# Kernel tuning notes

Measured on AMD Instinct MI355X. Metric: run time of the kernel, lower is better.

The kernel has to match this reference:

```python
import jax, jax.numpy as jnp
import numpy as np

SIGMA = 1.0
DELTA = 1.0
TOPK = 10
TOPK_HALF = 5  # int(np.around(TOPK / 2))
N, D = 4096, 512
N_IDS = 2048  # N / view


def _l2_normalize(x, eps=1e-12):
    n = jnp.linalg.norm(x, axis=1, keepdims=True)
    return x / jnp.maximum(n, eps)


def _cdist(a, b):
    # Euclidean distance with a sqrt that is safe at 0 (diagonal).
    sq = (jnp.sum(a * a, 1)[:, None] + jnp.sum(b * b, 1)[None, :]
          - 2.0 * (a @ b.T))
    sq = jnp.maximum(sq, 0.0)
    return jnp.where(sq > 0, jnp.sqrt(jnp.where(sq > 0, sq, 1.0)), 0.0)


def setup_inputs() -> dict:
    key = jax.random.key(0)
    k1, k2, k3 = jax.random.split(key, 3)
    s_emb = jax.random.normal(k1, (N, D), dtype=jnp.float32)
    t_emb = jax.random.normal(k2, (N, D), dtype=jnp.float32)
    idx = jax.random.randint(k3, (N,), 0, N_IDS, dtype=jnp.int64)
    return {"s_emb": s_emb, "t_emb": t_emb, "idx": idx}


def reference(s_emb, t_emb, idx):
    n = s_emb.shape[0]
    s = _l2_normalize(s_emb)          # disable_mu=True
    t = _l2_normalize(t_emb)

    S_dist = _cdist(s, s)
    S_dist = S_dist / jnp.mean(S_dist, axis=1, keepdims=True)

    # --- teacher-side neighbor graph (no_grad in original) ---
    T_dist = _cdist(t, t)
    W_P = jnp.exp(-(T_dist ** 2) / SIGMA)                      # [N,N]
    same = idx[:, None] == idx[None, :]
    W_P_copy = jnp.where(same, 1.0, W_P)
    _, topk_index = jax.lax.top_k(W_P_copy, TOPK)              # [N,k]
    topk_half_index = topk_index[:, :TOPK_HALF]                # [N,k/2]

    rows = jnp.arange(n)[:, None]
    W_NN = jnp.zeros((n, n), jnp.float32).at[rows, topk_index].set(1.0)
    V = ((W_NN + W_NN.T) / 2.0 == 1.0).astype(jnp.float32)     # mutual kNN

    # Vectorized form of the per-row nonzero gather-reduce loop:
    # W_C_tilda[i,j] = V[i,j] * (sum_l V[i,l] V[j,l]) / |{l: V[i,l]>0}|
    row_cnt = jnp.sum(V, axis=1)                               # [N]
    VV = jnp.einsum('il,jl->ij', V, V)                         # [N,N]
    W_C_tilda = jnp.where(V > 0, VV / jnp.maximum(row_cnt, 1.0)[:, None], 0.0)

    W_C_hat = jnp.mean(W_C_tilda[topk_half_index], axis=1)     # [N,k/2,N]->[N,N]
    W_C = (W_C_hat + W_C_hat.T) / 2.0
    W = (W_P + W_C) / 2.0

    eye = jnp.eye(n, dtype=jnp.float32)
    pos_weight = W * (1.0 - eye)
    neg_weight = (1.0 - W) * (1.0 - eye)

    pull = jnp.maximum(S_dist, 0.0) ** 2 * pos_weight
    push = jnp.maximum(DELTA - S_dist, 0.0) ** 2 * neg_weight
    loss = (jnp.sum(pull) + jnp.sum(push)) / (n * (n - 1))
    return loss
```

## Files before the change

### kernel.cpp

```cpp
#include <hip/hip_runtime.h>
#include <math.h>

#define N 4096
#define D 512
#define TOPK 10
#define TOPK_HALF 5
#define NT 32
#define TRI_BLOCKS (NT * (NT + 1) / 2)
#define WC_BLOCKS (N * TOPK_HALF / 16)
#define INV_N (1.0f / 4096.0f)
#define TPAD 132

typedef __bf16 bf16;
typedef __bf16 bf16x4 __attribute__((ext_vector_type(4)));
typedef __bf16 bf16x8 __attribute__((ext_vector_type(8)));
typedef float f32x4 __attribute__((ext_vector_type(4)));
typedef _Float16 f16;
typedef _Float16 f16x4 __attribute__((ext_vector_type(4)));
typedef _Float16 f16x8 __attribute__((ext_vector_type(8)));
typedef unsigned short u16;
typedef unsigned short u16x8 __attribute__((ext_vector_type(8)));
typedef unsigned int u32;

__device__ __forceinline__ void gl_lds16(const void* g, void* l) {
  __builtin_amdgcn_global_load_lds(
      (const __attribute__((address_space(1))) void*)g,
      (__attribute__((address_space(3))) void*)l, 16, 0, 0);
}

__device__ __forceinline__ float f16tof(u16 h) {
  return (float)__builtin_bit_cast(_Float16, h);
}

__global__ __launch_bounds__(256) void k_normalize2(const float* __restrict__ xs,
                                                    const float* __restrict__ xt,
                                                    bf16* __restrict__ ys,
                                                    bf16* __restrict__ yt,
                                                    float* __restrict__ rsq_s,
                                                    float* __restrict__ rsq_t,
                                                    float* __restrict__ rowsum) {
  int b = blockIdx.x;
  int tid = threadIdx.x;
  int half = tid >> 7;
  int l = tid & 127;
  int row2 = 2 * b + half;
  int is_t = row2 >> 12;
  int row = row2 & (N - 1);
  const float* x = is_t ? xt : xs;
  bf16* y = is_t ? yt : ys;
  float* rowsq = is_t ? rsq_t : rsq_s;
  const float* xr = x + (size_t)row * D;
  float4 v = *(const float4*)(xr + l * 4);
  float ss = v.x * v.x + v.y * v.y + v.z * v.z + v.w * v.w;
  __shared__ float red[4];
  __shared__ float red2[4];
  for (int off = 32; off > 0; off >>= 1) ss += __shfl_down(ss, off, 64);
  if ((tid & 63) == 0) red[tid >> 6] = ss;
  __syncthreads();
  float tot = red[half * 2] + red[half * 2 + 1];
  float inv = 1.0f / fmaxf(sqrtf(tot), 1e-12f);
  bf16x4 bv;
  bv[0] = (bf16)(v.x * inv); bv[1] = (bf16)(v.y * inv);
  bv[2] = (bf16)(v.z * inv); bv[3] = (bf16)(v.w * inv);
  *(bf16x4*)(y + (size_t)row * D + l * 4) = bv;
  float f0 = (float)bv[0], f1 = (float)bv[1], f2 = (float)bv[2], f3 = (float)bv[3];
  float s2 = f0 * f0 + f1 * f1 + f2 * f2 + f3 * f3;
  for (int off = 32; off > 0; off >>= 1) s2 += __shfl_down(s2, off, 64);
  if ((tid & 63) == 0) red2[tid >> 6] = s2;
  __syncthreads();
  if ((tid & 127) == 0) {
    rowsq[row] = red2[half * 2] + red2[half * 2 + 1];
    if (!is_t) rowsum[row] = 0.f;
  }
}

__global__ __launch_bounds__(256) void k_dgram3(const bf16* __restrict__ S,
                                                const bf16* __restrict__ T,
                                                const float* __restrict__ rsq_s,
                                                const float* __restrict__ rsq_t,
                                                f16* __restrict__ Gsd,
                                                f16* __restrict__ Gwp,
                                                float* __restrict__ rowsum) {
  __shared__ __align__(16) char sm[33792];
  f16* tp = (f16*)sm;

  int z = blockIdx.y;
  const bf16* Y = z ? T : S;
  const float* rsq = z ? rsq_t : rsq_s;
  f16* G = z ? Gwp : Gsd;

  int orig = blockIdx.x;
  int t = (orig & 7) * (TRI_BLOCKS / 8) + (orig >> 3);
  int by = 0;
  while (t >= NT - by) { t -= NT - by; ++by; }
  int bx = by + t;
  bool offdiag = (bx != by);

  int tid = threadIdx.x;
  int lane = tid & 63, w = tid >> 6;
  int wr = w >> 1, wc = w & 1;
  int quad = lane >> 4, c = lane & 15;

  const char* Jbase = (const char*)(Y + (size_t)(bx * 128) * D);
  const char* Ibase = (const char*)(Y + (size_t)(by * 128) * D);

  int goff[4];
  int ldso[4];
#pragma unroll
  for (int i = 0; i < 4; ++i) {
    int s = i * 256 + tid;
    int r = s >> 3;
    int cs = (tid & 7) ^ (r & 7);
    goff[i] = r * (D * 2) + cs * 16;
    ldso[i] = (i * 256 + w * 64) * 16;
  }

  int jrow = wr * 64 + c;
  int irow = wc * 64 + c;
  int x7 = c & 7;
  int csx0 = ((quad) ^ x7) * 16;
  int csx1 = ((4 + quad) ^ x7) * 16;

  f32x4 acc[4][4] = {};
  for (int tt = 0; tt < 8; ++tt) {
    int kb = tt * 128;
#pragma unroll
    for (int i = 0; i < 4; ++i) gl_lds16(Jbase + goff[i] + kb, sm + ldso[i]);
#pragma unroll
    for (int i = 0; i < 4; ++i) gl_lds16(Ibase + goff[i] + kb, sm + 16384 + ldso[i]);
    asm volatile("s_waitcnt vmcnt(0)\n\ts_barrier" ::: "memory");
    {
      const char* Jc = sm;
      const char* Ic = sm + 16384;
#pragma unroll
      for (int m = 0; m < 2; ++m) {
        int csx = m ? csx1 : csx0;
        bf16x8 af[4], bfr[4];
#pragma unroll
        for (int u = 0; u < 4; ++u)
          af[u] = *(const bf16x8*)(Jc + jrow * 128 + u * 2048 + csx);
#pragma unroll
        for (int v = 0; v < 4; ++v)
          bfr[v] = *(const bf16x8*)(Ic + irow * 128 + v * 2048 + csx);
#pragma unroll
        for (int u = 0; u < 4; ++u)
#pragma unroll
          for (int v = 0; v < 4; ++v)
            acc[u][v] = __builtin_amdgcn_mfma_f32_16x16x32_bf16(
                af[u], bfr[v], acc[u][v], 0, 0, 0);
      }
    }
    asm volatile("s_waitcnt lgkmcnt(0)\n\ts_barrier" ::: "memory");
  }

#pragma unroll
  for (int v = 0; v < 4; ++v) {
    int il = wc * 64 + v * 16 + c;
    int ig = by * 128 + il;
    float ri = rsq[ig];
    float rsv = 0.f;
#pragma unroll
    for (int u = 0; u < 4; ++u) {
      int jl0 = wr * 64 + u * 16 + quad * 4;
      int jb0i = bx * 128 + jl0;
      float4 rj = *(const float4*)(rsq + jb0i);
      const float* rjp = (const float*)&rj;
      f32x4 a = acc[u][v];
      f16x4 st;
      if (z == 0) {
#pragma unroll
        for (int reg = 0; reg < 4; ++reg) {
          float sq = fmaxf(ri + rjp[reg] - 2.0f * a[reg], 0.0f);
          float val = __builtin_amdgcn_sqrtf(sq);
          st[reg] = (_Float16)val;
          rsv += val;
        }
      } else {
#pragma unroll
        for (int reg = 0; reg < 4; ++reg) {
          float sq = fmaxf(ri + rjp[reg] - 2.0f * a[reg], 0.0f);
          st[reg] = (_Float16)__expf(-sq);
        }
      }
      *(f16x4*)(G + (size_t)ig * N + jb0i) = st;
      if (offdiag) {
#pragma unroll
        for (int reg = 0; reg < 4; ++reg) tp[(jl0 + reg) * TPAD + il] = st[reg];
      }
    }
    if (z == 0) {
      rsv += __shfl_xor(rsv, 16, 64);
      rsv += __shfl_xor(rsv, 32, 64);
      if (lane < 16) atomicAdd(&rowsum[ig], rsv);
    }
  }

  if (offdiag) {
    __syncthreads();
    int rloc = tid >> 4;
    int cseg = tid & 15;
#pragma unroll
    for (int it = 0; it < 8; ++it) {
      int jl = it * 16 + rloc;
      int jg = bx * 128 + jl;
      f16x8 v8 = *(f16x8*)&tp[jl * TPAD + cseg * 8];
      *(f16x8*)(G + (size_t)jg * N + by * 128 + cseg * 8) = v8;
      if (z == 0) {
        float csum = 0.f;
#pragma unroll
        for (int e = 0; e < 8; ++e) csum += (float)v8[e];
        csum += __shfl_xor(csum, 1, 64);
        csum += __shfl_xor(csum, 2, 64);
        csum += __shfl_xor(csum, 4, 64);
        csum += __shfl_xor(csum, 8, 64);
        if (cseg == 0) atomicAdd(&rowsum[jg], csum);
      }
    }
  }
}

__global__ __launch_bounds__(256) void k_rowpass(const f16* __restrict__ Gs,
                                                 const f16* __restrict__ Gw,
                                                 const int* __restrict__ ids,
                                                 const float* __restrict__ rowsum,
                                                 int* __restrict__ topk,
                                                 double* __restrict__ pd) {
  __shared__ u32 lds[256 * TOPK];
  __shared__ double dred[4];
  int i = blockIdx.x, tid = threadIdx.x;
  int idi = ids[i];
  float invm = 1.0f / (rowsum[i] * INV_N);
  const u16* srow = (const u16*)(Gs + (size_t)i * N);
  const u16* wrow = (const u16*)(Gw + (size_t)i * N);
  u32 key[16];
  float dsum = 0.f;
  int j0 = tid * 16;
#pragma unroll
  for (int h = 0; h < 2; ++h) {
    int jb = j0 + h * 8;
    u16x8 sv = *(const u16x8*)(srow + jb);
    u16x8 wv = *(const u16x8*)(wrow + jb);
    int4 id0 = *(const int4*)(ids + jb);
    int4 id1 = *(const int4*)(ids + jb + 4);
    const int* idp = (const int*)&id0;
    const int* idp1 = (const int*)&id1;
#pragma unroll
    for (int e = 0; e < 8; ++e) {
      int j = jb + e;
      u16 hw = wv[e];
      float wp = f16tof(hw);
      if (j != i) {
        float sdn = f16tof(sv[e]) * invm;
        float r = fmaxf(1.0f - sdn, 0.0f); r *= r;
        dsum += r + 0.5f * wp * (sdn * sdn - r);
      }
      int idj = (e < 4) ? idp[e] : idp1[e - 4];
      u16 hk = (idj == idi) ? (u16)0x3C00 : hw;
      key[h * 8 + e] = ((u32)hk << 16) | (u32)(4095 - j);
    }
  }
#pragma unroll
  for (int kk = 2; kk <= 16; kk <<= 1) {
#pragma unroll
    for (int jj = kk >> 1; jj > 0; jj >>= 1) {
#pragma unroll
      for (int ii = 0; ii < 16; ++ii) {
        int ll = ii ^ jj;
        if (ll > ii) {
          bool desc = ((ii & kk) == 0);
          u32 a = key[ii], b = key[ll];
          bool sw = desc ? (a < b) : (a > b);
          key[ii] = sw ? b : a;
          key[ll] = sw ? a : b;
        }
      }
    }
  }
  double dl = (double)dsum;
  for (int off = 32; off > 0; off >>= 1) dl += __shfl_down(dl, off, 64);
  if ((tid & 63) == 0) dred[tid >> 6] = dl;
#pragma unroll
  for (int o = 0; o < TOPK; ++o) lds[tid * TOPK + o] = key[o];
  __syncthreads();
  for (int off = 128; off >= 1; off >>= 1) {
    if (tid < off) {
      u32 A[TOPK], B[TOPK];
#pragma unroll
      for (int o = 0; o < TOPK; ++o) {
        A[o] = lds[tid * TOPK + o];
        B[o] = lds[(tid + off) * TOPK + o];
      }
      u32 out[TOPK];
#pragma unroll
      for (int o = 0; o < TOPK; ++o) {
        u32 m = A[o] > B[o] ? A[o] : B[o];
#pragma unroll
        for (int p = 0; p < o; ++p) {
          u32 mn = A[p] < B[o - 1 - p] ? A[p] : B[o - 1 - p];
          m = m > mn ? m : mn;
        }
        out[o] = m;
      }
#pragma unroll
      for (int o = 0; o < TOPK; ++o) lds[tid * TOPK + o] = out[o];
    }
    __syncthreads();
  }
  if (tid == 0) {
#pragma unroll
    for (int o = 0; o < TOPK; ++o)
      topk[i * TOPK + o] = 4095 - (int)(lds[o] & 0xFFFu);
    pd[i] = dred[0] + dred[1] + dred[2] + dred[3];
  }
}

__global__ __launch_bounds__(256) void k_buildV(const int* __restrict__ topk,
                                                int* __restrict__ L,
                                                int* __restrict__ cnt) {
  int tid = threadIdx.x;
  int grp = tid >> 4, gl = tid & 15;
  int i = blockIdx.x * 16 + grp;
  bool act = (gl < TOPK);
  int j = act ? topk[i * TOPK + gl] : 0;
  bool mut = false;
  if (act) {
#pragma unroll
    for (int q = 0; q < TOPK; ++q) mut |= (topk[j * TOPK + q] == i);
  }
  unsigned long long m = __ballot(mut);
  int base = tid & 48;
  unsigned gm = (unsigned)((m >> base) & 0xFFFFull);
  int pos = __popc(gm & ((1u << gl) - 1));
  if (mut) L[i * TOPK + pos] = j;
  if (gl == 0) cnt[i] = __popc(gm);
}

__global__ __launch_bounds__(256) void k_wc(const int* __restrict__ topk,
                                            const int* __restrict__ L,
                                            const int* __restrict__ cnt,
                                            const f16* __restrict__ Gsd,
                                            const float* __restrict__ rowsum,
                                            double* __restrict__ pw) {
  __shared__ double red[16];
  int tid = threadIdx.x;
  int grp = tid >> 4;
  int gl = tid & 15;
  int task = blockIdx.x * 16 + grp;
  int i = task / TOPK_HALF, m = task % TOPK_HALF;
  int r = topk[i * TOPK + m];
  int cr = cnt[r];
  float invmi = 1.0f / (rowsum[i] * INV_N);
  int lval = (gl < cr) ? L[r * TOPK + gl] : -1;
  int Lr[TOPK];
#pragma unroll
  for (int a = 0; a < TOPK; ++a) Lr[a] = __shfl(lval, a, 16);
  float contrib = 0.f;
  if (gl < cr) {
    int j = lval;
    if (j != i) {
      int cj = cnt[j];
      float mj = rowsum[j] * INV_N;
      float sr_ = f16tof(((const u16*)Gsd)[(size_t)i * N + j]);
      int lj[TOPK];
#pragma unroll
      for (int b = 0; b < TOPK; ++b) lj[b] = L[j * TOPK + b];
      int vv = 0;
#pragma unroll
      for (int b = 0; b < TOPK; ++b) {
        if (b < cj) {
#pragma unroll
          for (int a = 0; a < TOPK; ++a)
            vv += ((a < cr) && (lj[b] == Lr[a])) ? 1 : 0;
        }
      }
      float denom = (float)(cr > 1 ? cr : 1);
      float wgt = (float)vv / denom;
      float sdij = sr_ * invmi;
      float sdji = sr_ / mj;
      float Rij = fmaxf(1.0f - sdij, 0.0f); Rij *= Rij;
      float Rji = fmaxf(1.0f - sdji, 0.0f); Rji *= Rji;
      float Fij = sdij * sdij - Rij;
      float Fji = sdji * sdji - Rji;
      contrib = wgt * (Fij + Fji);
    }
  }
  double local = (double)contrib;
  local += __shfl_xor(local, 1, 16);
  local += __shfl_xor(local, 2, 16);
  local += __shfl_xor(local, 4, 16);
  local += __shfl_xor(local, 8, 16);
  if (gl == 0) red[grp] = local;
  __syncthreads();
  if (tid == 0) {
    double s = 0.0;
#pragma unroll
    for (int g = 0; g < 16; ++g) s += red[g];
    pw[blockIdx.x] = s * (1.0 / 20.0);
  }
}

__global__ __launch_bounds__(256) void k_final(const double* __restrict__ pd,
                                               const double* __restrict__ pw,
                                               float* __restrict__ out) {
  int tid = threadIdx.x;
  double s = 0.0;
  for (int i = tid; i < N; i += 256) s += pd[i];
  for (int i = tid; i < WC_BLOCKS; i += 256) s += pw[i];
  for (int off = 32; off > 0; off >>= 1) s += __shfl_down(s, off, 64);
  __shared__ double red[4];
  if ((tid & 63) == 0) red[tid >> 6] = s;
  __syncthreads();
  if (tid == 0)
    out[0] = (float)((red[0] + red[1] + red[2] + red[3]) /
                     ((double)N * (double)(N - 1)));
}

extern "C" void kernel_launch(void* const* d_in, const int* in_sizes, int n_in,
                              void* d_out, int out_size, void* d_ws, size_t ws_size,
                              hipStream_t stream) {
  const float* s_emb = (const float*)d_in[0];
  const float* t_emb = (const float*)d_in[1];
  const int* ids = (const int*)d_in[2];
  float* out = (float*)d_out;

  char* ws = (char*)d_ws;
  size_t off = 0;
  bf16* snorm = (bf16*)(ws + off); off += (size_t)N * D * 2;
  bf16* tnorm = (bf16*)(ws + off); off += (size_t)N * D * 2;
  f16*  Gsd   = (f16*)(ws + off);  off += (size_t)N * N * 2;
  f16*  Gwp   = (f16*)(ws + off);  off += (size_t)N * N * 2;
  float* rsq_s = (float*)(ws + off); off += (size_t)N * 4;
  float* rsq_t = (float*)(ws + off); off += (size_t)N * 4;
  float* rowsum= (float*)(ws + off); off += (size_t)N * 4;
  int*   topk  = (int*)(ws + off);   off += (size_t)N * TOPK * 4;
  int*   L     = (int*)(ws + off);   off += (size_t)N * TOPK * 4;
  int*   cnt   = (int*)(ws + off);   off += (size_t)N * 4;
  off = (off + 15) & ~(size_t)15;
  double* pd   = (double*)(ws + off); off += (size_t)N * 8;
  double* pw   = (double*)(ws + off); off += (size_t)WC_BLOCKS * 8;

  k_normalize2<<<N, 256, 0, stream>>>(s_emb, t_emb, snorm, tnorm,
                                      rsq_s, rsq_t, rowsum);
  k_dgram3<<<dim3(TRI_BLOCKS, 2), 256, 0, stream>>>(snorm, tnorm, rsq_s, rsq_t,
                                                    Gsd, Gwp, rowsum);
  k_rowpass<<<N, 256, 0, stream>>>(Gsd, Gwp, ids, rowsum, topk, pd);
  k_buildV<<<N / 16, 256, 0, stream>>>(topk, L, cnt);
  k_wc<<<WC_BLOCKS, 256, 0, stream>>>(topk, L, cnt, Gsd, rowsum, pw);
  k_final<<<1, 256, 0, stream>>>(pd, pw, out);
}
```

Measured before the change: 154.0 us.

## Enlarge Gram tiles to 256x256 with double-buffered LDS loads and 512 threads

The symmetric distance Gram kernel moves from 128x128 tiles (528 triangular blocks per matrix) to 256x256 tiles (136 blocks) run by 8 waves. Global-to-LDS loads are double-buffered so the next K-slice loads while MFMAs run on the current one. The transposed write-back is redone in two halves, recomputing values from the accumulators into LDS, because the larger tile's transpose buffer would not fit alongside. This cuts operand reloads and barrier stalls per output, but leaves only 272 blocks for the GPU, uses 128KB LDS per block, and raises register pressure from the doubled accumulators.

```diff
diff --git a/kernel.cpp b/kernel.cpp
--- a/kernel.cpp
+++ b/kernel.cpp
@@ -5,11 +5,11 @@
 #define D 512
 #define TOPK 10
 #define TOPK_HALF 5
-#define NT 32
-#define TRI_BLOCKS (NT * (NT + 1) / 2)
+#define NT2 16
+#define TRI2 (NT2 * (NT2 + 1) / 2)
 #define WC_BLOCKS (N * TOPK_HALF / 16)
 #define INV_N (1.0f / 4096.0f)
-#define TPAD 132
+#define TP2 260
 
 typedef __bf16 bf16;
 typedef __bf16 bf16x4 __attribute__((ext_vector_type(4)));
@@ -74,14 +74,14 @@
   }
 }
 
-__global__ __launch_bounds__(256) void k_dgram3(const bf16* __restrict__ S,
-                                                const bf16* __restrict__ T,
-                                                const float* __restrict__ rsq_s,
-                                                const float* __restrict__ rsq_t,
-                                                f16* __restrict__ Gsd,
-                                                f16* __restrict__ Gwp,
-                                                float* __restrict__ rowsum) {
-  __shared__ __align__(16) char sm[33792];
+__global__ __launch_bounds__(512, 2) void k_dgram4(const bf16* __restrict__ S,
+                                                   const bf16* __restrict__ T,
+                                                   const float* __restrict__ rsq_s,
+                                                   const float* __restrict__ rsq_t,
+                                                   f16* __restrict__ Gsd,
+                                                   f16* __restrict__ Gwp,
+                                                   float* __restrict__ rowsum) {
+  __shared__ __align__(16) char sm[131072];
   f16* tp = (f16*)sm;
 
   int z = blockIdx.y;
@@ -90,80 +90,81 @@
   f16* G = z ? Gwp : Gsd;
 
   int orig = blockIdx.x;
-  int t = (orig & 7) * (TRI_BLOCKS / 8) + (orig >> 3);
+  int t = (orig & 7) * (TRI2 / 8) + (orig >> 3);
   int by = 0;
-  while (t >= NT - by) { t -= NT - by; ++by; }
+  while (t >= NT2 - by) { t -= NT2 - by; ++by; }
   int bx = by + t;
   bool offdiag = (bx != by);
 
   int tid = threadIdx.x;
   int lane = tid & 63, w = tid >> 6;
-  int wr = w >> 1, wc = w & 1;
+  int wr = w >> 2, wc = w & 3;
   int quad = lane >> 4, c = lane & 15;
-
-  const char* Jbase = (const char*)(Y + (size_t)(bx * 128) * D);
-  const char* Ibase = (const char*)(Y + (size_t)(by * 128) * D);
-
-  int goff[4];
-  int ldso[4];
-#pragma unroll
-  for (int i = 0; i < 4; ++i) {
-    int s = i * 256 + tid;
-    int r = s >> 3;
-    int cs = (tid & 7) ^ (r & 7);
-    goff[i] = r * (D * 2) + cs * 16;
-    ldso[i] = (i * 256 + w * 64) * 16;
-  }
-
-  int jrow = wr * 64 + c;
-  int irow = wc * 64 + c;
   int x7 = c & 7;
-  int csx0 = ((quad) ^ x7) * 16;
-  int csx1 = ((4 + quad) ^ x7) * 16;
-
-  f32x4 acc[4][4] = {};
-  for (int tt = 0; tt < 8; ++tt) {
-    int kb = tt * 128;
-#pragma unroll
-    for (int i = 0; i < 4; ++i) gl_lds16(Jbase + goff[i] + kb, sm + ldso[i]);
-#pragma unroll
-    for (int i = 0; i < 4; ++i) gl_lds16(Ibase + goff[i] + kb, sm + 16384 + ldso[i]);
-    asm volatile("s_waitcnt vmcnt(0)\n\ts_barrier" ::: "memory");
-    {
-      const char* Jc = sm;
-      const char* Ic = sm + 16384;
-#pragma unroll
-      for (int m = 0; m < 2; ++m) {
-        int csx = m ? csx1 : csx0;
-        bf16x8 af[4], bfr[4];
-#pragma unroll
-        for (int u = 0; u < 4; ++u)
-          af[u] = *(const bf16x8*)(Jc + jrow * 128 + u * 2048 + csx);
-#pragma unroll
-        for (int v = 0; v < 4; ++v)
-          bfr[v] = *(const bf16x8*)(Ic + irow * 128 + v * 2048 + csx);
-#pragma unroll
-        for (int u = 0; u < 4; ++u)
-#pragma unroll
-          for (int v = 0; v < 4; ++v)
-            acc[u][v] = __builtin_amdgcn_mfma_f32_16x16x32_bf16(
-                af[u], bfr[v], acc[u][v], 0, 0, 0);
-      }
-    }
-    asm volatile("s_waitcnt lgkmcnt(0)\n\ts_barrier" ::: "memory");
-  }
+
+  const char* Jbase = (const char*)(Y + (size_t)(bx * 256) * D);
+  const char* Ibase = (const char*)(Y + (size_t)(by * 256) * D);
+
+  int r0 = tid >> 3;
+  int cs0 = (tid & 7) ^ (r0 & 7);
+  int goffb = r0 * 1024 + cs0 * 16;
+  int w1024 = w << 10;
+
+#define STG(buf, kb)                                                       \
+  {                                                                        \
+    char* _b = (buf);                                                      \
+    _Pragma("unroll") for (int i = 0; i < 4; ++i) {                        \
+      gl_lds16(Jbase + goffb + i * 65536 + (kb), _b + i * 8192 + w1024);   \
+      gl_lds16(Ibase + goffb + i * 65536 + (kb),                           \
+               _b + 32768 + i * 8192 + w1024);                             \
+    }                                                                      \
+  }
+
+#define CMP(bufc)                                                          \
+  {                                                                        \
+    const char* Jc = (const char*)(bufc);                                  \
+    const char* Ic = (const char*)(bufc) + 32768;                          \
+    _Pragma("unroll") for (int m = 0; m < 2; ++m) {                        \
+      int kx = ((m * 4 + quad) ^ x7) << 4;                                 \
+      bf16x8 af[8], bfr[4];                                                \
+      _Pragma("unroll") for (int u = 0; u < 8; ++u)                        \
+        af[u] = *(const bf16x8*)(Jc + (wr * 128 + u * 16 + c) * 128 + kx); \
+      _Pragma("unroll") for (int v = 0; v < 4; ++v)                        \
+        bfr[v] = *(const bf16x8*)(Ic + (wc * 64 + v * 16 + c) * 128 + kx); \
+      _Pragma("unroll") for (int u = 0; u < 8; ++u)                        \
+        _Pragma("unroll") for (int v = 0; v < 4; ++v)                      \
+          acc[u][v] = __builtin_amdgcn_mfma_f32_16x16x32_bf16(             \
+              af[u], bfr[v], acc[u][v], 0, 0, 0);                          \
+    }                                                                      \
+  }
+
+  f32x4 acc[8][4] = {};
+  STG(sm, 0);
+  for (int tt = 0; tt < 7; ++tt) {
+    asm volatile("s_barrier" ::: "memory");
+    STG(((tt + 1) & 1) ? (sm + 65536) : sm, (tt + 1) * 128);
+    asm volatile("s_waitcnt vmcnt(8)\n\ts_barrier" ::: "memory");
+    CMP((tt & 1) ? (sm + 65536) : sm);
+    asm volatile("s_waitcnt lgkmcnt(0)" ::: "memory");
+  }
+  asm volatile("s_waitcnt vmcnt(0)\n\ts_barrier" ::: "memory");
+  CMP(sm + 65536);
+  __syncthreads();
+
+#undef STG
+#undef CMP
 
 #pragma unroll
   for (int v = 0; v < 4; ++v) {
     int il = wc * 64 + v * 16 + c;
-    int ig = by * 128 + il;
+    int ig = by * 256 + il;
     float ri = rsq[ig];
     float rsv = 0.f;
 #pragma unroll
-    for (int u = 0; u < 4; ++u) {
-      int jl0 = wr * 64 + u * 16 + quad * 4;
-      int jb0i = bx * 128 + jl0;
-      float4 rj = *(const float4*)(rsq + jb0i);
+    for (int u = 0; u < 8; ++u) {
+      int jl0 = wr * 128 + u * 16 + quad * 4;
+      int jb = bx * 256 + jl0;
+      float4 rj = *(const float4*)(rsq + jb);
       const float* rjp = (const float*)&rj;
       f32x4 a = acc[u][v];
       f16x4 st;
@@ -182,11 +183,7 @@
           st[reg] = (_Float16)__expf(-sq);
         }
       }
-      *(f16x4*)(G + (size_t)ig * N + jb0i) = st;
-      if (offdiag) {
-#pragma unroll
-        for (int reg = 0; reg < 4; ++reg) tp[(jl0 + reg) * TPAD + il] = st[reg];
-      }
+      *(f16x4*)(G + (size_t)ig * N + jb) = st;
     }
     if (z == 0) {
       rsv += __shfl_xor(rsv, 16, 64);
@@ -196,24 +193,49 @@
   }
 
   if (offdiag) {
-    __syncthreads();
-    int rloc = tid >> 4;
-    int cseg = tid & 15;
-#pragma unroll
-    for (int it = 0; it < 8; ++it) {
-      int jl = it * 16 + rloc;
-      int jg = bx * 128 + jl;
-      f16x8 v8 = *(f16x8*)&tp[jl * TPAD + cseg * 8];
-      *(f16x8*)(G + (size_t)jg * N + by * 128 + cseg * 8) = v8;
-      if (z == 0) {
-        float csum = 0.f;
-#pragma unroll
-        for (int e = 0; e < 8; ++e) csum += (float)v8[e];
-        csum += __shfl_xor(csum, 1, 64);
-        csum += __shfl_xor(csum, 2, 64);
-        csum += __shfl_xor(csum, 4, 64);
-        csum += __shfl_xor(csum, 8, 64);
-        if (cseg == 0) atomicAdd(&rowsum[jg], csum);
+#pragma unroll
+    for (int h = 0; h < 2; ++h) {
+      __syncthreads();
+      if (wr == h) {
+#pragma unroll
+        for (int v = 0; v < 4; ++v) {
+          int il = wc * 64 + v * 16 + c;
+          float ri = rsq[by * 256 + il];
+#pragma unroll
+          for (int u = 0; u < 8; ++u) {
+            int jl0 = u * 16 + quad * 4;
+            float4 rj = *(const float4*)(rsq + bx * 256 + h * 128 + jl0);
+            const float* rjp = (const float*)&rj;
+            f32x4 a = acc[u][v];
+#pragma unroll
+            for (int reg = 0; reg < 4; ++reg) {
+              float sq = fmaxf(ri + rjp[reg] - 2.0f * a[reg], 0.0f);
+              tp[(jl0 + reg) * TP2 + il] =
+                  (z == 0) ? (_Float16)__builtin_amdgcn_sqrtf(sq)
+                           : (_Float16)__expf(-sq);
+            }
+          }
+        }
+      }
+      __syncthreads();
+      int rloc = tid >> 5, cseg = tid & 31;
+#pragma unroll
+      for (int p = 0; p < 8; ++p) {
+        int jlr = p * 16 + rloc;
+        int jg = bx * 256 + h * 128 + jlr;
+        f16x8 v8 = *(f16x8*)&tp[jlr * TP2 + cseg * 8];
+        *(f16x8*)(G + (size_t)jg * N + by * 256 + cseg * 8) = v8;
+        if (z == 0) {
+          float csum = 0.f;
+#pragma unroll
+          for (int e = 0; e < 8; ++e) csum += (float)v8[e];
+          csum += __shfl_xor(csum, 1, 64);
+          csum += __shfl_xor(csum, 2, 64);
+          csum += __shfl_xor(csum, 4, 64);
+          csum += __shfl_xor(csum, 8, 64);
+          csum += __shfl_xor(csum, 16, 64);
+          if (cseg == 0) atomicAdd(&rowsum[jg], csum);
+        }
       }
     }
   }
@@ -441,8 +463,8 @@
 
   k_normalize2<<<N, 256, 0, stream>>>(s_emb, t_emb, snorm, tnorm,
                                       rsq_s, rsq_t, rowsum);
-  k_dgram3<<<dim3(TRI_BLOCKS, 2), 256, 0, stream>>>(snorm, tnorm, rsq_s, rsq_t,
-                                                    Gsd, Gwp, rowsum);
+  k_dgram4<<<dim3(TRI2, 2), 512, 0, stream>>>(snorm, tnorm, rsq_s, rsq_t,
+                                              Gsd, Gwp, rowsum);
   k_rowpass<<<N, 256, 0, stream>>>(Gsd, Gwp, ids, rowsum, topk, pd);
   k_buildV<<<N / 16, 256, 0, stream>>>(topk, L, cnt);
   k_wc<<<WC_BLOCKS, 256, 0, stream>>>(topk, L, cnt, Gsd, rowsum, pw);
```

Measured after the change: 174.4 us. 1.13x slower.
